# Optimization experiments

Hardware: AMD Instinct MI355X
Metric: run time of the kernel (lower is better)

Reference implementation:

```python
import jax, jax.numpy as jnp
import numpy as np

N, D, C = 8192, 10000, 1000


def setup_inputs() -> dict:
    key = jax.random.key(0)
    k1, k2 = jax.random.split(key)
    # binary {0,1} hypervectors, stored as float32 for efficient GEMM-form Hamming distance
    samples = jax.random.randint(k1, (N, D), 0, 2).astype(jnp.float32)
    classes_hv = jax.random.randint(k2, (C, D), 0, 2).astype(jnp.float32)
    return {"samples": samples, "classes_hv": classes_hv}


def reference(samples, classes_hv):
    # Original: response[i] = sum_d xor(samples[:, d], classes_hv[i, d])  (Hamming distance)
    # For binary a,b: xor(a,b) = a + b - 2*a*b, so the full [N, C] distance matrix is
    # dist = row_sum(samples)[:, None] + row_sum(hv)[None, :] - 2 * samples @ hv.T
    # This replaces the per-class XOR+reduce loop with one GEMM (same math).
    s_sum = jnp.sum(samples, axis=-1)          # [N]
    c_sum = jnp.sum(classes_hv, axis=-1)       # [C]
    cross = jnp.einsum('nd,cd->nc', samples, classes_hv)  # [N, C]
    return s_sum[:, None] + c_sum[None, :] - 2.0 * cross  # [N, C] Hamming distances
```

## Files before the change

kernel.cpp:

```cpp
#include <hip/hip_runtime.h>
#include <stdint.h>

#define N_ROWS 8192
#define C_CLS  1000
#define D_DIM  10000
#define W64P   160
#define W32P   (W64P * 2)
#define BKW    16
#define NCHUNK 20

typedef int v4i  __attribute__((ext_vector_type(4)));
typedef int v16i __attribute__((ext_vector_type(16)));

__global__ __launch_bounds__(256) void pack_kernel(
    const float* __restrict__ samples, const float* __restrict__ classes,
    unsigned long long* __restrict__ pA, unsigned long long* __restrict__ pB,
    uint32_t* __restrict__ rsA, uint32_t* __restrict__ rsB)
{
    int gwave = (blockIdx.x * 256 + threadIdx.x) >> 6;
    int lane  = threadIdx.x & 63;
    if (gwave >= N_ROWS + C_CLS) return;

    const float* src;
    unsigned long long* dst;
    uint32_t* rsw;
    if (gwave < N_ROWS) {
        src = samples + (size_t)gwave * D_DIM;
        dst = pA + (size_t)gwave * W64P;
        rsw = rsA + gwave;
    } else {
        int r = gwave - N_ROWS;
        src = classes + (size_t)r * D_DIM;
        dst = pB + (size_t)r * W64P;
        rsw = rsB + r;
    }

    uint32_t rs = 0;
    #pragma unroll 4
    for (int w = 0; w < 40; ++w) {
        int idx = w * 256 + lane * 4;
        float4 v = make_float4(0.f, 0.f, 0.f, 0.f);
        if (idx < D_DIM) v = *(const float4*)(src + idx);
        unsigned long long m0 = __ballot(v.x > 0.5f);
        unsigned long long m1 = __ballot(v.y > 0.5f);
        unsigned long long m2 = __ballot(v.z > 0.5f);
        unsigned long long m3 = __ballot(v.w > 0.5f);
        rs += (uint32_t)(__popcll(m0) + __popcll(m1) + __popcll(m2) + __popcll(m3));
        if (lane == 0) {
            uint4 p0, p1;
            p0.x = (uint32_t)m0; p0.y = (uint32_t)(m0 >> 32);
            p0.z = (uint32_t)m1; p0.w = (uint32_t)(m1 >> 32);
            p1.x = (uint32_t)m2; p1.y = (uint32_t)(m2 >> 32);
            p1.z = (uint32_t)m3; p1.w = (uint32_t)(m3 >> 32);
            *(uint4*)(dst + (size_t)w * 4)     = p0;
            *(uint4*)(dst + (size_t)w * 4 + 2) = p1;
        }
    }
    if (lane == 0) *rsw = rs;
}

__global__ __launch_bounds__(256) void hd_kernel(
    const uint32_t* __restrict__ pA, const uint32_t* __restrict__ pB,
    const uint32_t* __restrict__ rsA, const uint32_t* __restrict__ rsB,
    float* __restrict__ out)
{
    __shared__ uint32_t AsT[2][BKW * 128];
    __shared__ uint32_t BsT[2][BKW * 128];

    const int tid  = threadIdx.x;
    const int row0 = blockIdx.x * 128;
    const int col0 = blockIdx.y * 128;

    const int w    = tid >> 6;
    const int lane = tid & 63;
    const int wy   = w >> 1;
    const int wx   = w & 1;
    const int ln   = lane & 31;
    const int h4   = (lane >> 5) * 4;

    const int srow = tid >> 1;
    const int sq2  = (tid & 1) * 2;
    const uint32_t* gAs = pA + (size_t)(row0 + srow) * W32P + sq2 * 4;
    int gc = col0 + srow; if (gc >= C_CLS) gc = C_CLS - 1;
    const uint32_t* gBs = pB + (size_t)gc * W32P + sq2 * 4;

    uint4 av[2], bv[2];

#define LOADR(ch) do {                                             \
    av[0] = *(const uint4*)(gAs + (ch) * BKW);                     \
    av[1] = *(const uint4*)(gAs + (ch) * BKW + 4);                 \
    bv[0] = *(const uint4*)(gBs + (ch) * BKW);                     \
    bv[1] = *(const uint4*)(gBs + (ch) * BKW + 4);                 \
} while (0)

#define WRITELDS(buf) do {                                         \
    uint32_t* ap_ = &AsT[buf][sq2 * 512 + srow * 2];               \
    uint32_t* bp_ = &BsT[buf][sq2 * 512 + srow * 2];               \
    *(uint2*)(ap_      ) = make_uint2(av[0].x, av[0].y);           \
    *(uint2*)(ap_ + 256) = make_uint2(av[0].z, av[0].w);           \
    *(uint2*)(ap_ + 512) = make_uint2(av[1].x, av[1].y);           \
    *(uint2*)(ap_ + 768) = make_uint2(av[1].z, av[1].w);           \
    *(uint2*)(bp_      ) = make_uint2(bv[0].x, bv[0].y);           \
    *(uint2*)(bp_ + 256) = make_uint2(bv[0].z, bv[0].w);           \
    *(uint2*)(bp_ + 512) = make_uint2(bv[1].x, bv[1].y);           \
    *(uint2*)(bp_ + 768) = make_uint2(bv[1].z, bv[1].w);           \
} while (0)

#define UNP(dst, src) do {                                         \
    dst[0] = (int)(((src) >> (h4 + 0)) & 0x01010101u);             \
    dst[1] = (int)(((src) >> (h4 + 1)) & 0x01010101u);             \
    dst[2] = (int)(((src) >> (h4 + 2)) & 0x01010101u);             \
    dst[3] = (int)(((src) >> (h4 + 3)) & 0x01010101u);             \
} while (0)

    v16i acc00 = {}, acc01 = {}, acc10 = {}, acc11 = {};

    LOADR(0);
    WRITELDS(0);
    __syncthreads();

    #pragma unroll 2
    for (int ch = 0; ch < NCHUNK; ++ch) {
        const int cur = ch & 1;
        if (ch + 1 < NCHUNK) LOADR(ch + 1);

        const uint32_t* Ac = &AsT[cur][0];
        const uint32_t* Bc = &BsT[cur][0];

        #pragma unroll
        for (int p = 0; p < BKW / 2; ++p) {
            uint2 wa0 = *(const uint2*)&Ac[p * 256 + (wy * 64 + ln) * 2];
            uint2 wa1 = *(const uint2*)&Ac[p * 256 + (wy * 64 + 32 + ln) * 2];
            uint2 wb0 = *(const uint2*)&Bc[p * 256 + (wx * 64 + ln) * 2];
            uint2 wb1 = *(const uint2*)&Bc[p * 256 + (wx * 64 + 32 + ln) * 2];
            v4i a0, a1, b0, b1;
            UNP(a0, wa0.x); UNP(a1, wa1.x); UNP(b0, wb0.x); UNP(b1, wb1.x);
            acc00 = __builtin_amdgcn_mfma_i32_32x32x32_i8(a0, b0, acc00, 0, 0, 0);
            acc01 = __builtin_amdgcn_mfma_i32_32x32x32_i8(a0, b1, acc01, 0, 0, 0);
            acc10 = __builtin_amdgcn_mfma_i32_32x32x32_i8(a1, b0, acc10, 0, 0, 0);
            acc11 = __builtin_amdgcn_mfma_i32_32x32x32_i8(a1, b1, acc11, 0, 0, 0);
            UNP(a0, wa0.y); UNP(a1, wa1.y); UNP(b0, wb0.y); UNP(b1, wb1.y);
            acc00 = __builtin_amdgcn_mfma_i32_32x32x32_i8(a0, b0, acc00, 0, 0, 0);
            acc01 = __builtin_amdgcn_mfma_i32_32x32x32_i8(a0, b1, acc01, 0, 0, 0);
            acc10 = __builtin_amdgcn_mfma_i32_32x32x32_i8(a1, b0, acc10, 0, 0, 0);
            acc11 = __builtin_amdgcn_mfma_i32_32x32x32_i8(a1, b1, acc11, 0, 0, 0);
        }

        if (ch + 1 < NCHUNK) {
            WRITELDS((ch + 1) & 1);
            __syncthreads();
        }
    }
#undef LOADR
#undef WRITELDS
#undef UNP

    const int gcol0 = col0 + wx * 64 + ln;
    const int gcol1 = gcol0 + 32;
    const uint32_t rb0 = (gcol0 < C_CLS) ? rsB[gcol0] : 0u;
    const uint32_t rb1 = (gcol1 < C_CLS) ? rsB[gcol1] : 0u;
    #pragma unroll
    for (int r = 0; r < 16; ++r) {
        const int m     = (r & 3) + 8 * (r >> 2) + h4;
        const int rowa  = row0 + wy * 64 + m;
        const int rowb  = rowa + 32;
        const uint32_t ra0 = rsA[rowa];
        const uint32_t ra1 = rsA[rowb];
        if (gcol0 < C_CLS) {
            out[(size_t)rowa * C_CLS + gcol0] =
                (float)(int)(ra0 + rb0 - 2u * (uint32_t)acc00[r]);
            out[(size_t)rowb * C_CLS + gcol0] =
                (float)(int)(ra1 + rb0 - 2u * (uint32_t)acc10[r]);
        }
        if (gcol1 < C_CLS) {
            out[(size_t)rowa * C_CLS + gcol1] =
                (float)(int)(ra0 + rb1 - 2u * (uint32_t)acc01[r]);
            out[(size_t)rowb * C_CLS + gcol1] =
                (float)(int)(ra1 + rb1 - 2u * (uint32_t)acc11[r]);
        }
    }
}

extern "C" void kernel_launch(void* const* d_in, const int* in_sizes, int n_in,
                              void* d_out, int out_size, void* d_ws, size_t ws_size,
                              hipStream_t stream) {
    const float* samples = (const float*)d_in[0];
    const float* classes = (const float*)d_in[1];
    float* out = (float*)d_out;

    unsigned long long* pA = (unsigned long long*)d_ws;
    unsigned long long* pB = pA + (size_t)N_ROWS * W64P;
    uint32_t* rsA = (uint32_t*)(pB + (size_t)C_CLS * W64P);
    uint32_t* rsB = rsA + N_ROWS;

    int waves  = N_ROWS + C_CLS;
    int blocks = (waves + 3) / 4;
    pack_kernel<<<blocks, 256, 0, stream>>>(samples, classes, pA, pB, rsA, rsB);

    dim3 grid(N_ROWS / 128, 8);
    hd_kernel<<<grid, 256, 0, stream>>>((const uint32_t*)pA, (const uint32_t*)pB,
                                        rsA, rsB, out);
}
```

Baseline: 543.6 us.

## Software-pipeline LDS reads, stagger k-slice order per wave, raise MFMA priority

The inner k-loop now double-buffers the LDS fragment reads in registers, prefetching slice i+1 while the MFMAs for slice i run. Each wave starts at a different k-slice offset (2*wave) so the four waves hit different LDS regions at the same time. MFMA groups are wrapped in s_setprio to favour matrix issue, and the unpack and MFMA calls are interleaved. The intent is to hide LDS latency and reduce bank contention, at the cost of more registers for the prefetched fragments.

```diff
diff --git a/kernel.cpp b/kernel.cpp
--- a/kernel.cpp
+++ b/kernel.cpp
@@ -64,8 +64,8 @@
     const uint32_t* __restrict__ rsA, const uint32_t* __restrict__ rsB,
     float* __restrict__ out)
 {
-    __shared__ uint32_t AsT[2][BKW * 128];
-    __shared__ uint32_t BsT[2][BKW * 128];
+    __shared__ uint32_t AsT[2][(BKW / 2) * 256];
+    __shared__ uint32_t BsT[2][(BKW / 2) * 256];
 
     const int tid  = threadIdx.x;
     const int row0 = blockIdx.x * 128;
@@ -77,6 +77,7 @@
     const int wx   = w & 1;
     const int ln   = lane & 31;
     const int h4   = (lane >> 5) * 4;
+    const int pb   = 2 * w;
 
     const int srow = tid >> 1;
     const int sq2  = (tid & 1) * 2;
@@ -95,11 +96,11 @@
 
 #define WRITELDS(buf) do {                                         \
     uint32_t* ap_ = &AsT[buf][sq2 * 512 + srow * 2];               \
-    uint32_t* bp_ = &BsT[buf][sq2 * 512 + srow * 2];               \
     *(uint2*)(ap_      ) = make_uint2(av[0].x, av[0].y);           \
     *(uint2*)(ap_ + 256) = make_uint2(av[0].z, av[0].w);           \
     *(uint2*)(ap_ + 512) = make_uint2(av[1].x, av[1].y);           \
     *(uint2*)(ap_ + 768) = make_uint2(av[1].z, av[1].w);           \
+    uint32_t* bp_ = &BsT[buf][sq2 * 512 + srow * 2];               \
     *(uint2*)(bp_      ) = make_uint2(bv[0].x, bv[0].y);           \
     *(uint2*)(bp_ + 256) = make_uint2(bv[0].z, bv[0].w);           \
     *(uint2*)(bp_ + 512) = make_uint2(bv[1].x, bv[1].y);           \
@@ -113,6 +114,24 @@
     dst[3] = (int)(((src) >> (h4 + 3)) & 0x01010101u);             \
 } while (0)
 
+#define STEP(wa0_, wa1_, wb0_, wb1_) do {                          \
+    v4i a0_, a1_, b0_, b1_;                                        \
+    UNP(a0_, wa0_); UNP(b0_, wb0_);                                \
+    acc00 = __builtin_amdgcn_mfma_i32_32x32x32_i8(a0_, b0_, acc00, 0, 0, 0); \
+    UNP(b1_, wb1_);                                                \
+    acc01 = __builtin_amdgcn_mfma_i32_32x32x32_i8(a0_, b1_, acc01, 0, 0, 0); \
+    UNP(a1_, wa1_);                                                \
+    acc10 = __builtin_amdgcn_mfma_i32_32x32x32_i8(a1_, b0_, acc10, 0, 0, 0); \
+    acc11 = __builtin_amdgcn_mfma_i32_32x32x32_i8(a1_, b1_, acc11, 0, 0, 0); \
+} while (0)
+
+#define LOADP(set, p) do {                                         \
+    ra0[set] = *(const uint2*)&Ac[(p) * 256 + (wy * 64 + ln) * 2];        \
+    ra1[set] = *(const uint2*)&Ac[(p) * 256 + (wy * 64 + 32 + ln) * 2];   \
+    rb0[set] = *(const uint2*)&Bc[(p) * 256 + (wx * 64 + ln) * 2];        \
+    rb1[set] = *(const uint2*)&Bc[(p) * 256 + (wx * 64 + 32 + ln) * 2];   \
+} while (0)
+
     v16i acc00 = {}, acc01 = {}, acc10 = {}, acc11 = {};
 
     LOADR(0);
@@ -127,23 +146,17 @@
         const uint32_t* Ac = &AsT[cur][0];
         const uint32_t* Bc = &BsT[cur][0];
 
+        uint2 ra0[2], ra1[2], rb0[2], rb1[2];
+        LOADP(0, pb & 7);
+
         #pragma unroll
-        for (int p = 0; p < BKW / 2; ++p) {
-            uint2 wa0 = *(const uint2*)&Ac[p * 256 + (wy * 64 + ln) * 2];
-            uint2 wa1 = *(const uint2*)&Ac[p * 256 + (wy * 64 + 32 + ln) * 2];
-            uint2 wb0 = *(const uint2*)&Bc[p * 256 + (wx * 64 + ln) * 2];
-            uint2 wb1 = *(const uint2*)&Bc[p * 256 + (wx * 64 + 32 + ln) * 2];
-            v4i a0, a1, b0, b1;
-            UNP(a0, wa0.x); UNP(a1, wa1.x); UNP(b0, wb0.x); UNP(b1, wb1.x);
-            acc00 = __builtin_amdgcn_mfma_i32_32x32x32_i8(a0, b0, acc00, 0, 0, 0);
-            acc01 = __builtin_amdgcn_mfma_i32_32x32x32_i8(a0, b1, acc01, 0, 0, 0);
-            acc10 = __builtin_amdgcn_mfma_i32_32x32x32_i8(a1, b0, acc10, 0, 0, 0);
-            acc11 = __builtin_amdgcn_mfma_i32_32x32x32_i8(a1, b1, acc11, 0, 0, 0);
-            UNP(a0, wa0.y); UNP(a1, wa1.y); UNP(b0, wb0.y); UNP(b1, wb1.y);
-            acc00 = __builtin_amdgcn_mfma_i32_32x32x32_i8(a0, b0, acc00, 0, 0, 0);
-            acc01 = __builtin_amdgcn_mfma_i32_32x32x32_i8(a0, b1, acc01, 0, 0, 0);
-            acc10 = __builtin_amdgcn_mfma_i32_32x32x32_i8(a1, b0, acc10, 0, 0, 0);
-            acc11 = __builtin_amdgcn_mfma_i32_32x32x32_i8(a1, b1, acc11, 0, 0, 0);
+        for (int i = 0; i < 8; ++i) {
+            const int c = i & 1, n = c ^ 1;
+            if (i < 7) LOADP(n, (pb + i + 1) & 7);
+            __builtin_amdgcn_s_setprio(1);
+            STEP(ra0[c].x, ra1[c].x, rb0[c].x, rb1[c].x);
+            STEP(ra0[c].y, ra1[c].y, rb0[c].y, rb1[c].y);
+            __builtin_amdgcn_s_setprio(0);
         }
 
         if (ch + 1 < NCHUNK) {
@@ -154,29 +167,31 @@
 #undef LOADR
 #undef WRITELDS
 #undef UNP
+#undef STEP
+#undef LOADP
 
     const int gcol0 = col0 + wx * 64 + ln;
     const int gcol1 = gcol0 + 32;
-    const uint32_t rb0 = (gcol0 < C_CLS) ? rsB[gcol0] : 0u;
-    const uint32_t rb1 = (gcol1 < C_CLS) ? rsB[gcol1] : 0u;
+    const uint32_t rb0v = (gcol0 < C_CLS) ? rsB[gcol0] : 0u;
+    const uint32_t rb1v = (gcol1 < C_CLS) ? rsB[gcol1] : 0u;
     #pragma unroll
     for (int r = 0; r < 16; ++r) {
-        const int m     = (r & 3) + 8 * (r >> 2) + h4;
-        const int rowa  = row0 + wy * 64 + m;
-        const int rowb  = rowa + 32;
-        const uint32_t ra0 = rsA[rowa];
-        const uint32_t ra1 = rsA[rowb];
+        const int m    = (r & 3) + 8 * (r >> 2) + h4;
+        const int rowa = row0 + wy * 64 + m;
+        const int rowb = rowa + 32;
+        const uint32_t ra0v = rsA[rowa];
+        const uint32_t ra1v = rsA[rowb];
         if (gcol0 < C_CLS) {
             out[(size_t)rowa * C_CLS + gcol0] =
-                (float)(int)(ra0 + rb0 - 2u * (uint32_t)acc00[r]);
+                (float)(int)(ra0v + rb0v - 2u * (uint32_t)acc00[r]);
             out[(size_t)rowb * C_CLS + gcol0] =
-                (float)(int)(ra1 + rb0 - 2u * (uint32_t)acc10[r]);
+                (float)(int)(ra1v + rb0v - 2u * (uint32_t)acc10[r]);
         }
         if (gcol1 < C_CLS) {
             out[(size_t)rowa * C_CLS + gcol1] =
-                (float)(int)(ra0 + rb1 - 2u * (uint32_t)acc01[r]);
+                (float)(int)(ra0v + rb1v - 2u * (uint32_t)acc01[r]);
             out[(size_t)rowb * C_CLS + gcol1] =
-                (float)(int)(ra1 + rb1 - 2u * (uint32_t)acc11[r]);
+                (float)(int)(ra1v + rb1v - 2u * (uint32_t)acc11[r]);
         }
     }
 }
```

Result: no change. 543.6 us (+0.0%).
